# Kernel optimization log

Measured on AMD Instinct MI355X. Metric: run time of the kernel, lower is better.

Reference implementation:

```python
import jax, jax.numpy as jnp
import numpy as np

ALPHA = 0.2  # LeakyReLU negative slope

def setup_inputs() -> dict:
    key = jax.random.key(0)
    k1, k2, k3 = jax.random.split(key, 3)
    B, N, IN_DIM = 16, 1024, 128
    HEADS, HEAD_DIM = 2, 64  # out_dim = 128
    h = jax.random.normal(k1, (B, N, IN_DIM), dtype=jnp.float32)
    # xavier_uniform with gain=1.414 ~ uniform(-b, b); exact init unimportant for correctness
    bW = 1.414 * np.sqrt(6.0 / (IN_DIM + HEAD_DIM))
    W = jax.random.uniform(k2, (HEADS, IN_DIM, HEAD_DIM), minval=-bW, maxval=bW, dtype=jnp.float32)
    ba = 1.414 * np.sqrt(6.0 / (2 * HEAD_DIM + 1))
    a = jax.random.uniform(k3, (HEADS, 2 * HEAD_DIM, 1), minval=-ba, maxval=ba, dtype=jnp.float32)
    return {"h": h, "W": W, "a": a}

def reference(h, W, a):
    B, N, in_dim = h.shape
    heads, _, head_dim = W.shape
    out_dim = heads * head_dim
    # h_prime: [B, N, H, D]
    hp = jnp.einsum('bni,hio->bnho', h, W)
    # Split additive attention: a . [h_i ; h_j] = a_src . h_i + a_dst . h_j (same math as concat)
    a_src = a[:, :head_dim, 0]   # [H, D]
    a_dst = a[:, head_dim:, 0]   # [H, D]
    e_src = jnp.einsum('bnhd,hd->bhn', hp, a_src)  # [B, H, N]
    e_dst = jnp.einsum('bmhd,hd->bhm', hp, a_dst)  # [B, H, N]
    e = e_src[:, :, :, None] + e_dst[:, :, None, :]  # [B, H, N, N]
    e = jnp.where(e >= 0, e, ALPHA * e)  # LeakyReLU(0.2)
    att = jax.nn.softmax(e, axis=-1)
    # dropout p=0.0 (eval-deterministic): no-op
    h_new = jnp.einsum('bhnm,bmho->bnho', att, hp).reshape(B, N, out_dim)
    out = h_new + h if in_dim == out_dim else h_new
    return jax.nn.elu(out)
```

## Files before the change

kernel.cpp:

```cpp
#include <hip/hip_runtime.h>
#include <math.h>


#define LOG2E 1.44269504088896340736f

typedef __bf16 bf16x8 __attribute__((ext_vector_type(8)));
typedef float floatx4 __attribute__((ext_vector_type(4)));

union U16x8 { uint4 u; bf16x8 b; };

__device__ __forceinline__ unsigned short f2bf(float f) {
    union { __bf16 b; unsigned short u; } x;
    x.b = (__bf16)f;
    return x.u;
}

__global__ __launch_bounds__(256) void gat_prep(
    const float* __restrict__ Wg,
    const float* __restrict__ ag,
    unsigned short* __restrict__ Wp,
    float* __restrict__ acat)
{
    const int t = threadIdx.x;
    const int base = blockIdx.x * 1024;
#pragma unroll
    for (int i = 0; i < 4; ++i) {
        int idx = base + i * 256 + t;
        int c = idx & 127, k = idx >> 7;
        float v = Wg[(c >> 6) * 8192 + k * 64 + (c & 63)];
        Wp[((k >> 3) * 128 + c) * 8 + (k & 7)] = f2bf(v);
    }
    if (blockIdx.x == 0 && t < 128) {
        acat[t]       = ag[(t >> 6) * 128 + (t & 63)];
        acat[128 + t] = ag[(t >> 6) * 128 + 64 + (t & 63)];
    }
}

__global__ __launch_bounds__(256) void gat_hp(
    const float* __restrict__ hg,
    const unsigned short* __restrict__ Wp,
    const float* __restrict__ acat,
    unsigned short* __restrict__ hpB,
    float* __restrict__ es_g,
    float* __restrict__ ed_g,
    float* __restrict__ e1_g,
    float* __restrict__ e5_g)
{
    const int t = threadIdx.x;
    const int lane = t & 63;
    const int wv = blockIdx.x * 4 + (t >> 6);
    const int rt = wv >> 1;
    const int half = wv & 1;
    const int n0 = rt * 16;
    const int col = lane & 15, quad = lane >> 4;

    floatx4 acc[4];
#pragma unroll
    for (int ct = 0; ct < 4; ++ct) acc[ct] = (floatx4){0.f, 0.f, 0.f, 0.f};

    const float* hrow = hg + (size_t)(n0 + col) * 128;
    const uint4* wp4 = (const uint4*)Wp;
#pragma unroll
    for (int kq = 0; kq < 4; ++kq) {
        float4 h0 = *(const float4*)(hrow + kq * 32 + quad * 8);
        float4 h1 = *(const float4*)(hrow + kq * 32 + quad * 8 + 4);
        bf16x8 af;
        af[0] = (__bf16)h0.x; af[1] = (__bf16)h0.y;
        af[2] = (__bf16)h0.z; af[3] = (__bf16)h0.w;
        af[4] = (__bf16)h1.x; af[5] = (__bf16)h1.y;
        af[6] = (__bf16)h1.z; af[7] = (__bf16)h1.w;
        const uint4* wbase = wp4 + (size_t)(kq * 4 + quad) * 128 + half * 64;
#pragma unroll
        for (int ct = 0; ct < 4; ++ct) {
            U16x8 bu; bu.u = wbase[ct * 16 + col];
            acc[ct] = __builtin_amdgcn_mfma_f32_16x16x32_bf16(af, bu.b, acc[ct], 0, 0, 0);
        }
    }

    const int b = n0 >> 10;
    const int nloc = n0 & 1023;
    const int bh = b * 2 + half;

    float esr[4] = {0.f, 0.f, 0.f, 0.f}, edr[4] = {0.f, 0.f, 0.f, 0.f};
#pragma unroll
    for (int ct = 0; ct < 4; ++ct) {
        int c = half * 64 + ct * 16 + col;
        float as = acat[c], ad = acat[128 + c];
#pragma unroll
        for (int r = 0; r < 4; ++r) {
            esr[r] = fmaf(acc[ct][r], as, esr[r]);
            edr[r] = fmaf(acc[ct][r], ad, edr[r]);
        }
    }
#pragma unroll
    for (int off = 1; off <= 8; off <<= 1) {
#pragma unroll
        for (int r = 0; r < 4; ++r) {
            esr[r] += __shfl_xor(esr[r], off, 64);
            edr[r] += __shfl_xor(edr[r], off, 64);
        }
    }
    if (col == 0) {
        size_t base = (size_t)bh * 1024 + nloc + quad * 4;
#pragma unroll
        for (int r = 0; r < 4; ++r) {
            es_g[base + r] = esr[r];
            ed_g[base + r] = edr[r];
            e1_g[base + r] = __builtin_amdgcn_exp2f(edr[r] * LOG2E);
            e5_g[base + r] = __builtin_amdgcn_exp2f(edr[r] * (0.2f * LOG2E));
        }
    }

    const int gloc = (nloc >> 3) + (quad >> 1);
#pragma unroll
    for (int ct = 0; ct < 4; ++ct) {
        int d = ct * 16 + col;
        uint2 pk;
        pk.x = (unsigned)f2bf(acc[ct][0]) | ((unsigned)f2bf(acc[ct][1]) << 16);
        pk.y = (unsigned)f2bf(acc[ct][2]) | ((unsigned)f2bf(acc[ct][3]) << 16);
        size_t idx = ((size_t)(bh * 128 + gloc) * 64 + d) * 8 + (quad & 1) * 4;
        *(uint2*)(hpB + idx) = pk;
    }
}

__global__ __launch_bounds__(256, 2) void gat_att(
    const float* __restrict__ hg,
    const unsigned short* __restrict__ hpB,
    const float* __restrict__ es_g,
    const float* __restrict__ ed_g,
    const float* __restrict__ e1_g,
    const float* __restrict__ e5_g,
    float* __restrict__ out)
{
    __shared__ float red[4 * 64 * 35];

    const int t = threadIdx.x;
    const int lane = t & 63;
    const int w = t >> 6;
    const int bh = blockIdx.x & 31;
    const int nt = blockIdx.x >> 5;
    const int b = bh >> 1, hh = bh & 1;
    const int n0 = nt * 32;
    const int col = lane & 15, quad = lane >> 4;

    const float* edrow = ed_g + (size_t)bh * 1024;
    const float* e1row = e1_g + (size_t)bh * 1024;
    const float* e5row = e5_g + (size_t)bh * 1024;

    float mx = -1e30f;
#pragma unroll
    for (int i = 0; i < 4; ++i) {
        float4 v = *(const float4*)(edrow + lane * 16 + i * 4);
        mx = fmaxf(mx, fmaxf(fmaxf(v.x, v.y), fmaxf(v.z, v.w)));
    }
#pragma unroll
    for (int off = 1; off < 64; off <<= 1) mx = fmaxf(mx, __shfl_xor(mx, off, 64));
    const float mxl = mx * LOG2E;

    const float s2a = es_g[(size_t)bh * 1024 + n0 + col] * LOG2E;
    const float s2b = es_g[(size_t)bh * 1024 + n0 + 16 + col] * LOG2E;
    const float x0a = s2a + mxl, x0b = s2b + mxl;
    const float Ma = fmaxf(x0a, 0.2f * x0a), Mb = fmaxf(x0b, 0.2f * x0b);
    const float C2a = __builtin_amdgcn_exp2f(s2a - Ma);
    const float C5a = __builtin_amdgcn_exp2f(0.2f * s2a - Ma);
    const float C2b = __builtin_amdgcn_exp2f(s2b - Mb);
    const float C5b = __builtin_amdgcn_exp2f(0.2f * s2b - Mb);

    floatx4 acc0[4], acc1[4];
#pragma unroll
    for (int ct = 0; ct < 4; ++ct) {
        acc0[ct] = (floatx4){0.f, 0.f, 0.f, 0.f};
        acc1[ct] = (floatx4){0.f, 0.f, 0.f, 0.f};
    }
    float ls0 = 0.f, ls1 = 0.f;

    const uint4* hb = (const uint4*)hpB + (size_t)bh * 8192;
    const int mbase = w * 256;

    float4 d0 = *(const float4*)(e1row + mbase + quad * 8);
    float4 d1 = *(const float4*)(e1row + mbase + quad * 8 + 4);
    float4 f0 = *(const float4*)(e5row + mbase + quad * 8);
    float4 f1 = *(const float4*)(e5row + mbase + quad * 8 + 4);
    int gm = (mbase >> 3) + quad;
    uint4 bu0 = hb[gm * 64 + col];
    uint4 bu1 = hb[gm * 64 + 16 + col];
    uint4 bu2 = hb[gm * 64 + 32 + col];
    uint4 bu3 = hb[gm * 64 + 48 + col];

#pragma unroll
    for (int i = 0; i < 8; ++i) {
        float4 c0 = d0, c1 = d1, g0 = f0, g1 = f1;
        uint4 cb0 = bu0, cb1 = bu1, cb2 = bu2, cb3 = bu3;
        if (i < 7) {
            int m1 = mbase + (i + 1) * 32;
            d0 = *(const float4*)(e1row + m1 + quad * 8);
            d1 = *(const float4*)(e1row + m1 + quad * 8 + 4);
            f0 = *(const float4*)(e5row + m1 + quad * 8);
            f1 = *(const float4*)(e5row + m1 + quad * 8 + 4);
            gm = (m1 >> 3) + quad;
            bu0 = hb[gm * 64 + col];
            bu1 = hb[gm * 64 + 16 + col];
            bu2 = hb[gm * 64 + 32 + col];
            bu3 = hb[gm * 64 + 48 + col];
        }
        float ev[8] = {c0.x, c0.y, c0.z, c0.w, c1.x, c1.y, c1.z, c1.w};
        float fv[8] = {g0.x, g0.y, g0.z, g0.w, g1.x, g1.y, g1.z, g1.w};
        bf16x8 af0, af1;
#pragma unroll
        for (int j = 0; j < 8; ++j) {
            float pa = fmaxf(ev[j] * C2a, fv[j] * C5a);
            float pb = fmaxf(ev[j] * C2b, fv[j] * C5b);
            ls0 += pa; ls1 += pb;
            af0[j] = (__bf16)pa;
            af1[j] = (__bf16)pb;
        }
        U16x8 u0; u0.u = cb0;
        U16x8 u1; u1.u = cb1;
        U16x8 u2; u2.u = cb2;
        U16x8 u3; u3.u = cb3;
        acc0[0] = __builtin_amdgcn_mfma_f32_16x16x32_bf16(af0, u0.b, acc0[0], 0, 0, 0);
        acc1[0] = __builtin_amdgcn_mfma_f32_16x16x32_bf16(af1, u0.b, acc1[0], 0, 0, 0);
        acc0[1] = __builtin_amdgcn_mfma_f32_16x16x32_bf16(af0, u1.b, acc0[1], 0, 0, 0);
        acc1[1] = __builtin_amdgcn_mfma_f32_16x16x32_bf16(af1, u1.b, acc1[1], 0, 0, 0);
        acc0[2] = __builtin_amdgcn_mfma_f32_16x16x32_bf16(af0, u2.b, acc0[2], 0, 0, 0);
        acc1[2] = __builtin_amdgcn_mfma_f32_16x16x32_bf16(af1, u2.b, acc1[2], 0, 0, 0);
        acc0[3] = __builtin_amdgcn_mfma_f32_16x16x32_bf16(af0, u3.b, acc0[3], 0, 0, 0);
        acc1[3] = __builtin_amdgcn_mfma_f32_16x16x32_bf16(af1, u3.b, acc1[3], 0, 0, 0);
    }

    ls0 += __shfl_xor(ls0, 16, 64); ls0 += __shfl_xor(ls0, 32, 64);
    ls1 += __shfl_xor(ls1, 16, 64); ls1 += __shfl_xor(ls1, 32, 64);

    float* myred = red + (w * 64 + lane) * 35;
#pragma unroll
    for (int ct = 0; ct < 4; ++ct)
#pragma unroll
        for (int r = 0; r < 4; ++r) {
            myred[ct * 4 + r]      = acc0[ct][r];
            myred[16 + ct * 4 + r] = acc1[ct][r];
        }
    myred[32] = ls0;
    myred[33] = ls1;
    __syncthreads();

    const int tile = w & 1;
    const int ctp = w >> 1;
    float ltot = 0.f;
#pragma unroll
    for (int v4 = 0; v4 < 4; ++v4)
        ltot += red[(v4 * 64 + lane) * 35 + 32 + tile];
    float inv[4];
#pragma unroll
    for (int r = 0; r < 4; ++r)
        inv[r] = __builtin_amdgcn_rcpf(__shfl(ltot, quad * 4 + r, 16));

#pragma unroll
    for (int cti = 0; cti < 2; ++cti) {
        const int ct = ctp * 2 + cti;
        float facc[4] = {0.f, 0.f, 0.f, 0.f};
#pragma unroll
        for (int v4 = 0; v4 < 4; ++v4) {
            const float* rr = red + (v4 * 64 + lane) * 35 + tile * 16 + ct * 4;
#pragma unroll
            for (int r = 0; r < 4; ++r) facc[r] += rr[r];
        }
#pragma unroll
        for (int r = 0; r < 4; ++r) {
            int n = n0 + tile * 16 + quad * 4 + r;
            size_t off = (size_t)(b * 1024 + n) * 128 + hh * 64 + ct * 16 + col;
            float vv = facc[r] * inv[r] + hg[off];
            out[off] = vv > 0.f ? vv : __builtin_amdgcn_exp2f(vv * LOG2E) - 1.f;
        }
    }
}

extern "C" void kernel_launch(void* const* d_in, const int* in_sizes, int n_in,
                              void* d_out, int out_size, void* d_ws, size_t ws_size,
                              hipStream_t stream) {
    const float* h = (const float*)d_in[0];
    const float* W = (const float*)d_in[1];
    const float* a = (const float*)d_in[2];
    float* out = (float*)d_out;

    unsigned short* hpB = (unsigned short*)d_ws;
    float* es  = (float*)((char*)d_ws + (4u << 20));
    float* ed  = es + 32 * 1024;
    float* e1  = ed + 32 * 1024;
    float* e5  = e1 + 32 * 1024;
    unsigned short* Wp = (unsigned short*)(e5 + 32 * 1024);
    float* acat = (float*)((char*)Wp + 16384 * sizeof(unsigned short));

    gat_prep<<<16, 256, 0, stream>>>(W, a, Wp, acat);
    gat_hp<<<512, 256, 0, stream>>>(h, Wp, acat, hpB, es, ed, e1, e5);
    gat_att<<<1024, 256, 0, stream>>>(h, hpB, es, ed, e1, e5, out);
}
```

Baseline: 84.35 us.

## Fuse prep, projection and attention into one persistent kernel with grid barrier

Replaces the three-kernel pipeline with a single 512-block kernel. Each block converts W to bf16 in LDS, computes its share of the projected features and the attention scores, then waits at a global atomic barrier built from magic flag values before each block handles two attention tiles. This removes two kernel launches and the launch gaps between stages, and W is read from LDS instead of a global prep buffer. In exchange every block redoes the W conversion, and correctness depends on all 512 blocks being resident at once; if they are not, the spin barrier can deadlock.

```diff
diff --git a/kernel.cpp b/kernel.cpp
--- a/kernel.cpp
+++ b/kernel.cpp
@@ -3,6 +3,8 @@
 
 
 #define LOG2E 1.44269504088896340736f
+#define MAGIC_READY 0x1F2E3D4Cu
+#define MAGIC_GO    0x600DF00Du
 
 typedef __bf16 bf16x8 __attribute__((ext_vector_type(8)));
 typedef float floatx4 __attribute__((ext_vector_type(4)));
@@ -15,261 +17,271 @@
     return x.u;
 }
 
-__global__ __launch_bounds__(256) void gat_prep(
+__global__ __launch_bounds__(256, 2) void gat_fused(
+    const float* __restrict__ hg,
     const float* __restrict__ Wg,
     const float* __restrict__ ag,
-    unsigned short* __restrict__ Wp,
-    float* __restrict__ acat)
-{
-    const int t = threadIdx.x;
-    const int base = blockIdx.x * 1024;
-#pragma unroll
-    for (int i = 0; i < 4; ++i) {
-        int idx = base + i * 256 + t;
-        int c = idx & 127, k = idx >> 7;
-        float v = Wg[(c >> 6) * 8192 + k * 64 + (c & 63)];
-        Wp[((k >> 3) * 128 + c) * 8 + (k & 7)] = f2bf(v);
-    }
-    if (blockIdx.x == 0 && t < 128) {
-        acat[t]       = ag[(t >> 6) * 128 + (t & 63)];
-        acat[128 + t] = ag[(t >> 6) * 128 + 64 + (t & 63)];
-    }
-}
-
-__global__ __launch_bounds__(256) void gat_hp(
-    const float* __restrict__ hg,
-    const unsigned short* __restrict__ Wp,
-    const float* __restrict__ acat,
     unsigned short* __restrict__ hpB,
     float* __restrict__ es_g,
     float* __restrict__ ed_g,
     float* __restrict__ e1_g,
-    float* __restrict__ e5_g)
+    float* __restrict__ e5_g,
+    float* __restrict__ out,
+    unsigned* __restrict__ gsync)
 {
-    const int t = threadIdx.x;
-    const int lane = t & 63;
-    const int wv = blockIdx.x * 4 + (t >> 6);
-    const int rt = wv >> 1;
-    const int half = wv & 1;
-    const int n0 = rt * 16;
-    const int col = lane & 15, quad = lane >> 4;
-
-    floatx4 acc[4];
-#pragma unroll
-    for (int ct = 0; ct < 4; ++ct) acc[ct] = (floatx4){0.f, 0.f, 0.f, 0.f};
-
-    const float* hrow = hg + (size_t)(n0 + col) * 128;
-    const uint4* wp4 = (const uint4*)Wp;
-#pragma unroll
-    for (int kq = 0; kq < 4; ++kq) {
-        float4 h0 = *(const float4*)(hrow + kq * 32 + quad * 8);
-        float4 h1 = *(const float4*)(hrow + kq * 32 + quad * 8 + 4);
-        bf16x8 af;
-        af[0] = (__bf16)h0.x; af[1] = (__bf16)h0.y;
-        af[2] = (__bf16)h0.z; af[3] = (__bf16)h0.w;
-        af[4] = (__bf16)h1.x; af[5] = (__bf16)h1.y;
-        af[6] = (__bf16)h1.z; af[7] = (__bf16)h1.w;
-        const uint4* wbase = wp4 + (size_t)(kq * 4 + quad) * 128 + half * 64;
-#pragma unroll
-        for (int ct = 0; ct < 4; ++ct) {
-            U16x8 bu; bu.u = wbase[ct * 16 + col];
-            acc[ct] = __builtin_amdgcn_mfma_f32_16x16x32_bf16(af, bu.b, acc[ct], 0, 0, 0);
-        }
-    }
-
-    const int b = n0 >> 10;
-    const int nloc = n0 & 1023;
-    const int bh = b * 2 + half;
-
-    float esr[4] = {0.f, 0.f, 0.f, 0.f}, edr[4] = {0.f, 0.f, 0.f, 0.f};
-#pragma unroll
-    for (int ct = 0; ct < 4; ++ct) {
-        int c = half * 64 + ct * 16 + col;
-        float as = acat[c], ad = acat[128 + c];
-#pragma unroll
-        for (int r = 0; r < 4; ++r) {
-            esr[r] = fmaf(acc[ct][r], as, esr[r]);
-            edr[r] = fmaf(acc[ct][r], ad, edr[r]);
-        }
-    }
-#pragma unroll
-    for (int off = 1; off <= 8; off <<= 1) {
-#pragma unroll
-        for (int r = 0; r < 4; ++r) {
-            esr[r] += __shfl_xor(esr[r], off, 64);
-            edr[r] += __shfl_xor(edr[r], off, 64);
-        }
-    }
-    if (col == 0) {
-        size_t base = (size_t)bh * 1024 + nloc + quad * 4;
-#pragma unroll
-        for (int r = 0; r < 4; ++r) {
-            es_g[base + r] = esr[r];
-            ed_g[base + r] = edr[r];
-            e1_g[base + r] = __builtin_amdgcn_exp2f(edr[r] * LOG2E);
-            e5_g[base + r] = __builtin_amdgcn_exp2f(edr[r] * (0.2f * LOG2E));
-        }
-    }
-
-    const int gloc = (nloc >> 3) + (quad >> 1);
-#pragma unroll
-    for (int ct = 0; ct < 4; ++ct) {
-        int d = ct * 16 + col;
-        uint2 pk;
-        pk.x = (unsigned)f2bf(acc[ct][0]) | ((unsigned)f2bf(acc[ct][1]) << 16);
-        pk.y = (unsigned)f2bf(acc[ct][2]) | ((unsigned)f2bf(acc[ct][3]) << 16);
-        size_t idx = ((size_t)(bh * 128 + gloc) * 64 + d) * 8 + (quad & 1) * 4;
-        *(uint2*)(hpB + idx) = pk;
-    }
-}
-
-__global__ __launch_bounds__(256, 2) void gat_att(
-    const float* __restrict__ hg,
-    const unsigned short* __restrict__ hpB,
-    const float* __restrict__ es_g,
-    const float* __restrict__ ed_g,
-    const float* __restrict__ e1_g,
-    const float* __restrict__ e5_g,
-    float* __restrict__ out)
-{
-    __shared__ float red[4 * 64 * 35];
+    __shared__ float smem[4 * 64 * 35];
 
     const int t = threadIdx.x;
     const int lane = t & 63;
     const int w = t >> 6;
-    const int bh = blockIdx.x & 31;
-    const int nt = blockIdx.x >> 5;
-    const int b = bh >> 1, hh = bh & 1;
-    const int n0 = nt * 32;
     const int col = lane & 15, quad = lane >> 4;
 
-    const float* edrow = ed_g + (size_t)bh * 1024;
-    const float* e1row = e1_g + (size_t)bh * 1024;
-    const float* e5row = e5_g + (size_t)bh * 1024;
-
-    float mx = -1e30f;
-#pragma unroll
-    for (int i = 0; i < 4; ++i) {
-        float4 v = *(const float4*)(edrow + lane * 16 + i * 4);
-        mx = fmaxf(mx, fmaxf(fmaxf(v.x, v.y), fmaxf(v.z, v.w)));
-    }
-#pragma unroll
-    for (int off = 1; off < 64; off <<= 1) mx = fmaxf(mx, __shfl_xor(mx, off, 64));
-    const float mxl = mx * LOG2E;
-
-    const float s2a = es_g[(size_t)bh * 1024 + n0 + col] * LOG2E;
-    const float s2b = es_g[(size_t)bh * 1024 + n0 + 16 + col] * LOG2E;
-    const float x0a = s2a + mxl, x0b = s2b + mxl;
-    const float Ma = fmaxf(x0a, 0.2f * x0a), Mb = fmaxf(x0b, 0.2f * x0b);
-    const float C2a = __builtin_amdgcn_exp2f(s2a - Ma);
-    const float C5a = __builtin_amdgcn_exp2f(0.2f * s2a - Ma);
-    const float C2b = __builtin_amdgcn_exp2f(s2b - Mb);
-    const float C5b = __builtin_amdgcn_exp2f(0.2f * s2b - Mb);
-
-    floatx4 acc0[4], acc1[4];
-#pragma unroll
-    for (int ct = 0; ct < 4; ++ct) {
-        acc0[ct] = (floatx4){0.f, 0.f, 0.f, 0.f};
-        acc1[ct] = (floatx4){0.f, 0.f, 0.f, 0.f};
-    }
-    float ls0 = 0.f, ls1 = 0.f;
-
-    const uint4* hb = (const uint4*)hpB + (size_t)bh * 8192;
-    const int mbase = w * 256;
-
-    float4 d0 = *(const float4*)(e1row + mbase + quad * 8);
-    float4 d1 = *(const float4*)(e1row + mbase + quad * 8 + 4);
-    float4 f0 = *(const float4*)(e5row + mbase + quad * 8);
-    float4 f1 = *(const float4*)(e5row + mbase + quad * 8 + 4);
-    int gm = (mbase >> 3) + quad;
-    uint4 bu0 = hb[gm * 64 + col];
-    uint4 bu1 = hb[gm * 64 + 16 + col];
-    uint4 bu2 = hb[gm * 64 + 32 + col];
-    uint4 bu3 = hb[gm * 64 + 48 + col];
-
-#pragma unroll
-    for (int i = 0; i < 8; ++i) {
-        float4 c0 = d0, c1 = d1, g0 = f0, g1 = f1;
-        uint4 cb0 = bu0, cb1 = bu1, cb2 = bu2, cb3 = bu3;
-        if (i < 7) {
-            int m1 = mbase + (i + 1) * 32;
-            d0 = *(const float4*)(e1row + m1 + quad * 8);
-            d1 = *(const float4*)(e1row + m1 + quad * 8 + 4);
-            f0 = *(const float4*)(e5row + m1 + quad * 8);
-            f1 = *(const float4*)(e5row + m1 + quad * 8 + 4);
-            gm = (m1 >> 3) + quad;
-            bu0 = hb[gm * 64 + col];
-            bu1 = hb[gm * 64 + 16 + col];
-            bu2 = hb[gm * 64 + 32 + col];
-            bu3 = hb[gm * 64 + 48 + col];
-        }
-        float ev[8] = {c0.x, c0.y, c0.z, c0.w, c1.x, c1.y, c1.z, c1.w};
-        float fv[8] = {g0.x, g0.y, g0.z, g0.w, g1.x, g1.y, g1.z, g1.w};
-        bf16x8 af0, af1;
-#pragma unroll
-        for (int j = 0; j < 8; ++j) {
-            float pa = fmaxf(ev[j] * C2a, fv[j] * C5a);
-            float pb = fmaxf(ev[j] * C2b, fv[j] * C5b);
-            ls0 += pa; ls1 += pb;
-            af0[j] = (__bf16)pa;
-            af1[j] = (__bf16)pb;
-        }
-        U16x8 u0; u0.u = cb0;
-        U16x8 u1; u1.u = cb1;
-        U16x8 u2; u2.u = cb2;
-        U16x8 u3; u3.u = cb3;
-        acc0[0] = __builtin_amdgcn_mfma_f32_16x16x32_bf16(af0, u0.b, acc0[0], 0, 0, 0);
-        acc1[0] = __builtin_amdgcn_mfma_f32_16x16x32_bf16(af1, u0.b, acc1[0], 0, 0, 0);
-        acc0[1] = __builtin_amdgcn_mfma_f32_16x16x32_bf16(af0, u1.b, acc0[1], 0, 0, 0);
-        acc1[1] = __builtin_amdgcn_mfma_f32_16x16x32_bf16(af1, u1.b, acc1[1], 0, 0, 0);
-        acc0[2] = __builtin_amdgcn_mfma_f32_16x16x32_bf16(af0, u2.b, acc0[2], 0, 0, 0);
-        acc1[2] = __builtin_amdgcn_mfma_f32_16x16x32_bf16(af1, u2.b, acc1[2], 0, 0, 0);
-        acc0[3] = __builtin_amdgcn_mfma_f32_16x16x32_bf16(af0, u3.b, acc0[3], 0, 0, 0);
-        acc1[3] = __builtin_amdgcn_mfma_f32_16x16x32_bf16(af1, u3.b, acc1[3], 0, 0, 0);
-    }
-
-    ls0 += __shfl_xor(ls0, 16, 64); ls0 += __shfl_xor(ls0, 32, 64);
-    ls1 += __shfl_xor(ls1, 16, 64); ls1 += __shfl_xor(ls1, 32, 64);
-
-    float* myred = red + (w * 64 + lane) * 35;
-#pragma unroll
-    for (int ct = 0; ct < 4; ++ct)
-#pragma unroll
-        for (int r = 0; r < 4; ++r) {
-            myred[ct * 4 + r]      = acc0[ct][r];
-            myred[16 + ct * 4 + r] = acc1[ct][r];
-        }
-    myred[32] = ls0;
-    myred[33] = ls1;
+    if (blockIdx.x == 0 && t == 0) {
+        __hip_atomic_store(&gsync[0], 0u, __ATOMIC_RELAXED, __HIP_MEMORY_SCOPE_AGENT);
+        __hip_atomic_store(&gsync[1], MAGIC_READY, __ATOMIC_RELEASE, __HIP_MEMORY_SCOPE_AGENT);
+    }
+
+    {
+        unsigned short* Wlds = (unsigned short*)smem;
+#pragma unroll 4
+        for (int i = 0; i < 64; ++i) {
+            int idx = i * 256 + t;
+            int c = idx & 127, k = idx >> 7;
+            float v = Wg[(c >> 6) * 8192 + k * 64 + (c & 63)];
+            Wlds[((k >> 3) * 128 + c) * 8 + (k & 7)] = f2bf(v);
+        }
+    }
     __syncthreads();
 
-    const int tile = w & 1;
-    const int ctp = w >> 1;
-    float ltot = 0.f;
-#pragma unroll
-    for (int v4 = 0; v4 < 4; ++v4)
-        ltot += red[(v4 * 64 + lane) * 35 + 32 + tile];
-    float inv[4];
-#pragma unroll
-    for (int r = 0; r < 4; ++r)
-        inv[r] = __builtin_amdgcn_rcpf(__shfl(ltot, quad * 4 + r, 16));
-
-#pragma unroll
-    for (int cti = 0; cti < 2; ++cti) {
-        const int ct = ctp * 2 + cti;
-        float facc[4] = {0.f, 0.f, 0.f, 0.f};
-#pragma unroll
-        for (int v4 = 0; v4 < 4; ++v4) {
-            const float* rr = red + (v4 * 64 + lane) * 35 + tile * 16 + ct * 4;
-#pragma unroll
-            for (int r = 0; r < 4; ++r) facc[r] += rr[r];
-        }
-#pragma unroll
-        for (int r = 0; r < 4; ++r) {
-            int n = n0 + tile * 16 + quad * 4 + r;
-            size_t off = (size_t)(b * 1024 + n) * 128 + hh * 64 + ct * 16 + col;
-            float vv = facc[r] * inv[r] + hg[off];
-            out[off] = vv > 0.f ? vv : __builtin_amdgcn_exp2f(vv * LOG2E) - 1.f;
+    {
+        const int wv = blockIdx.x * 4 + w;
+        const int rt = wv >> 1;
+        const int half = wv & 1;
+        const int n0 = rt * 16;
+
+        floatx4 acc[4];
+#pragma unroll
+        for (int ct = 0; ct < 4; ++ct) acc[ct] = (floatx4){0.f, 0.f, 0.f, 0.f};
+
+        const float* hrow = hg + (size_t)(n0 + col) * 128;
+        const uint4* wl4 = (const uint4*)smem;
+#pragma unroll
+        for (int kq = 0; kq < 4; ++kq) {
+            float4 h0 = *(const float4*)(hrow + kq * 32 + quad * 8);
+            float4 h1 = *(const float4*)(hrow + kq * 32 + quad * 8 + 4);
+            bf16x8 af;
+            af[0] = (__bf16)h0.x; af[1] = (__bf16)h0.y;
+            af[2] = (__bf16)h0.z; af[3] = (__bf16)h0.w;
+            af[4] = (__bf16)h1.x; af[5] = (__bf16)h1.y;
+            af[6] = (__bf16)h1.z; af[7] = (__bf16)h1.w;
+            const uint4* wbase = wl4 + (kq * 4 + quad) * 128 + half * 64;
+#pragma unroll
+            for (int ct = 0; ct < 4; ++ct) {
+                U16x8 bu; bu.u = wbase[ct * 16 + col];
+                acc[ct] = __builtin_amdgcn_mfma_f32_16x16x32_bf16(af, bu.b, acc[ct], 0, 0, 0);
+            }
+        }
+
+        const int b = n0 >> 10;
+        const int nloc = n0 & 1023;
+        const int bh = b * 2 + half;
+
+        float esr[4] = {0.f, 0.f, 0.f, 0.f}, edr[4] = {0.f, 0.f, 0.f, 0.f};
+#pragma unroll
+        for (int ct = 0; ct < 4; ++ct) {
+            int dd = ct * 16 + col;
+            float as = ag[half * 128 + dd];
+            float ad = ag[half * 128 + 64 + dd];
+#pragma unroll
+            for (int r = 0; r < 4; ++r) {
+                esr[r] = fmaf(acc[ct][r], as, esr[r]);
+                edr[r] = fmaf(acc[ct][r], ad, edr[r]);
+            }
+        }
+#pragma unroll
+        for (int off = 1; off <= 8; off <<= 1) {
+#pragma unroll
+            for (int r = 0; r < 4; ++r) {
+                esr[r] += __shfl_xor(esr[r], off, 64);
+                edr[r] += __shfl_xor(edr[r], off, 64);
+            }
+        }
+        if (col == 0) {
+            size_t base = (size_t)bh * 1024 + nloc + quad * 4;
+#pragma unroll
+            for (int r = 0; r < 4; ++r) {
+                es_g[base + r] = esr[r];
+                ed_g[base + r] = edr[r];
+                e1_g[base + r] = __builtin_amdgcn_exp2f(edr[r] * LOG2E);
+                e5_g[base + r] = __builtin_amdgcn_exp2f(edr[r] * (0.2f * LOG2E));
+            }
+        }
+
+        const int gloc = (nloc >> 3) + (quad >> 1);
+#pragma unroll
+        for (int ct = 0; ct < 4; ++ct) {
+            int d = ct * 16 + col;
+            uint2 pk;
+            pk.x = (unsigned)f2bf(acc[ct][0]) | ((unsigned)f2bf(acc[ct][1]) << 16);
+            pk.y = (unsigned)f2bf(acc[ct][2]) | ((unsigned)f2bf(acc[ct][3]) << 16);
+            size_t idx = ((size_t)(bh * 128 + gloc) * 64 + d) * 8 + (quad & 1) * 4;
+            *(uint2*)(hpB + idx) = pk;
+        }
+    }
+
+    __syncthreads();
+    if (t == 0) {
+        __threadfence();
+        while (__hip_atomic_load(&gsync[1], __ATOMIC_ACQUIRE, __HIP_MEMORY_SCOPE_AGENT) != MAGIC_READY) {}
+        unsigned v = __hip_atomic_fetch_add(&gsync[0], 1u, __ATOMIC_ACQ_REL, __HIP_MEMORY_SCOPE_AGENT);
+        if (v == 511u) {
+            __hip_atomic_store(&gsync[1], MAGIC_GO, __ATOMIC_RELEASE, __HIP_MEMORY_SCOPE_AGENT);
+        } else {
+            while (__hip_atomic_load(&gsync[1], __ATOMIC_ACQUIRE, __HIP_MEMORY_SCOPE_AGENT) != MAGIC_GO)
+                __builtin_amdgcn_s_sleep(2);
+        }
+    }
+    __syncthreads();
+
+    {
+        const int bh = blockIdx.x & 31;
+        const int nt0 = blockIdx.x >> 5;
+        const int b = bh >> 1, hh = bh & 1;
+
+        const float* edrow = ed_g + (size_t)bh * 1024;
+        const float* e1row = e1_g + (size_t)bh * 1024;
+        const float* e5row = e5_g + (size_t)bh * 1024;
+        const uint4* hb = (const uint4*)hpB + (size_t)bh * 8192;
+        const int mbase = w * 256;
+        float* red = smem;
+
+        float mx = -1e30f;
+#pragma unroll
+        for (int i = 0; i < 4; ++i) {
+            float4 v = *(const float4*)(edrow + lane * 16 + i * 4);
+            mx = fmaxf(mx, fmaxf(fmaxf(v.x, v.y), fmaxf(v.z, v.w)));
+        }
+#pragma unroll
+        for (int off = 1; off < 64; off <<= 1) mx = fmaxf(mx, __shfl_xor(mx, off, 64));
+        const float mxl = mx * LOG2E;
+
+#pragma unroll 1
+        for (int u = 0; u < 2; ++u) {
+            const int n0 = (nt0 + u * 16) * 32;
+            __syncthreads();
+
+            const float s2a = es_g[(size_t)bh * 1024 + n0 + col] * LOG2E;
+            const float s2b = es_g[(size_t)bh * 1024 + n0 + 16 + col] * LOG2E;
+            const float x0a = s2a + mxl, x0b = s2b + mxl;
+            const float Ma = fmaxf(x0a, 0.2f * x0a), Mb = fmaxf(x0b, 0.2f * x0b);
+            const float C2a = __builtin_amdgcn_exp2f(s2a - Ma);
+            const float C5a = __builtin_amdgcn_exp2f(0.2f * s2a - Ma);
+            const float C2b = __builtin_amdgcn_exp2f(s2b - Mb);
+            const float C5b = __builtin_amdgcn_exp2f(0.2f * s2b - Mb);
+
+            floatx4 acc0[4], acc1[4];
+#pragma unroll
+            for (int ct = 0; ct < 4; ++ct) {
+                acc0[ct] = (floatx4){0.f, 0.f, 0.f, 0.f};
+                acc1[ct] = (floatx4){0.f, 0.f, 0.f, 0.f};
+            }
+            float ls0 = 0.f, ls1 = 0.f;
+
+            float4 d0 = *(const float4*)(e1row + mbase + quad * 8);
+            float4 d1 = *(const float4*)(e1row + mbase + quad * 8 + 4);
+            float4 f0 = *(const float4*)(e5row + mbase + quad * 8);
+            float4 f1 = *(const float4*)(e5row + mbase + quad * 8 + 4);
+            int gm = (mbase >> 3) + quad;
+            uint4 bu0 = hb[gm * 64 + col];
+            uint4 bu1 = hb[gm * 64 + 16 + col];
+            uint4 bu2 = hb[gm * 64 + 32 + col];
+            uint4 bu3 = hb[gm * 64 + 48 + col];
+
+#pragma unroll
+            for (int i = 0; i < 8; ++i) {
+                float4 c0 = d0, c1 = d1, g0 = f0, g1 = f1;
+                uint4 cb0 = bu0, cb1 = bu1, cb2 = bu2, cb3 = bu3;
+                if (i < 7) {
+                    int m1 = mbase + (i + 1) * 32;
+                    d0 = *(const float4*)(e1row + m1 + quad * 8);
+                    d1 = *(const float4*)(e1row + m1 + quad * 8 + 4);
+                    f0 = *(const float4*)(e5row + m1 + quad * 8);
+                    f1 = *(const float4*)(e5row + m1 + quad * 8 + 4);
+                    gm = (m1 >> 3) + quad;
+                    bu0 = hb[gm * 64 + col];
+                    bu1 = hb[gm * 64 + 16 + col];
+                    bu2 = hb[gm * 64 + 32 + col];
+                    bu3 = hb[gm * 64 + 48 + col];
+                }
+                float ev[8] = {c0.x, c0.y, c0.z, c0.w, c1.x, c1.y, c1.z, c1.w};
+                float fv[8] = {g0.x, g0.y, g0.z, g0.w, g1.x, g1.y, g1.z, g1.w};
+                bf16x8 af0, af1;
+#pragma unroll
+                for (int j = 0; j < 8; ++j) {
+                    float pa = fmaxf(ev[j] * C2a, fv[j] * C5a);
+                    float pb = fmaxf(ev[j] * C2b, fv[j] * C5b);
+                    ls0 += pa; ls1 += pb;
+                    af0[j] = (__bf16)pa;
+                    af1[j] = (__bf16)pb;
+                }
+                U16x8 u0; u0.u = cb0;
+                U16x8 u1; u1.u = cb1;
+                U16x8 u2; u2.u = cb2;
+                U16x8 u3; u3.u = cb3;
+                acc0[0] = __builtin_amdgcn_mfma_f32_16x16x32_bf16(af0, u0.b, acc0[0], 0, 0, 0);
+                acc1[0] = __builtin_amdgcn_mfma_f32_16x16x32_bf16(af1, u0.b, acc1[0], 0, 0, 0);
+                acc0[1] = __builtin_amdgcn_mfma_f32_16x16x32_bf16(af0, u1.b, acc0[1], 0, 0, 0);
+                acc1[1] = __builtin_amdgcn_mfma_f32_16x16x32_bf16(af1, u1.b, acc1[1], 0, 0, 0);
+                acc0[2] = __builtin_amdgcn_mfma_f32_16x16x32_bf16(af0, u2.b, acc0[2], 0, 0, 0);
+                acc1[2] = __builtin_amdgcn_mfma_f32_16x16x32_bf16(af1, u2.b, acc1[2], 0, 0, 0);
+                acc0[3] = __builtin_amdgcn_mfma_f32_16x16x32_bf16(af0, u3.b, acc0[3], 0, 0, 0);
+                acc1[3] = __builtin_amdgcn_mfma_f32_16x16x32_bf16(af1, u3.b, acc1[3], 0, 0, 0);
+            }
+
+            ls0 += __shfl_xor(ls0, 16, 64); ls0 += __shfl_xor(ls0, 32, 64);
+            ls1 += __shfl_xor(ls1, 16, 64); ls1 += __shfl_xor(ls1, 32, 64);
+
+            float* myred = red + (w * 64 + lane) * 35;
+#pragma unroll
+            for (int ct = 0; ct < 4; ++ct)
+#pragma unroll
+                for (int r = 0; r < 4; ++r) {
+                    myred[ct * 4 + r]      = acc0[ct][r];
+                    myred[16 + ct * 4 + r] = acc1[ct][r];
+                }
+            myred[32] = ls0;
+            myred[33] = ls1;
+            __syncthreads();
+
+            const int tile = w & 1;
+            const int ctp = w >> 1;
+            float ltot = 0.f;
+#pragma unroll
+            for (int v4 = 0; v4 < 4; ++v4)
+                ltot += red[(v4 * 64 + lane) * 35 + 32 + tile];
+            float inv[4];
+#pragma unroll
+            for (int r = 0; r < 4; ++r)
+                inv[r] = __builtin_amdgcn_rcpf(__shfl(ltot, quad * 4 + r, 16));
+
+#pragma unroll
+            for (int cti = 0; cti < 2; ++cti) {
+                const int ct = ctp * 2 + cti;
+                float facc[4] = {0.f, 0.f, 0.f, 0.f};
+#pragma unroll
+                for (int v4 = 0; v4 < 4; ++v4) {
+                    const float* rr = red + (v4 * 64 + lane) * 35 + tile * 16 + ct * 4;
+#pragma unroll
+                    for (int r = 0; r < 4; ++r) facc[r] += rr[r];
+                }
+#pragma unroll
+                for (int r = 0; r < 4; ++r) {
+                    int n = n0 + tile * 16 + quad * 4 + r;
+                    size_t off = (size_t)(b * 1024 + n) * 128 + hh * 64 + ct * 16 + col;
+                    float vv = facc[r] * inv[r] + hg[off];
+                    out[off] = vv > 0.f ? vv : __builtin_amdgcn_exp2f(vv * LOG2E) - 1.f;
+                }
+            }
         }
     }
 }
@@ -287,10 +299,7 @@
     float* ed  = es + 32 * 1024;
     float* e1  = ed + 32 * 1024;
     float* e5  = e1 + 32 * 1024;
-    unsigned short* Wp = (unsigned short*)(e5 + 32 * 1024);
-    float* acat = (float*)((char*)Wp + 16384 * sizeof(unsigned short));
-
-    gat_prep<<<16, 256, 0, stream>>>(W, a, Wp, acat);
-    gat_hp<<<512, 256, 0, stream>>>(h, Wp, acat, hpB, es, ed, e1, e5);
-    gat_att<<<1024, 256, 0, stream>>>(h, hpB, es, ed, e1, e5, out);
+    unsigned* gsync = (unsigned*)(e5 + 32 * 1024);
+
+    gat_fused<<<512, 256, 0, stream>>>(h, W, a, hpB, es, ed, e1, e5, out, gsync);
 }
```

Result: slower. 143.0 us (+69.6%).
